# Performance work log

Hardware: AMD Instinct MI355X
Metric: run time of the kernel (lower is better)

The kernel has to match this reference:

```python
import jax, jax.numpy as jnp
import numpy as np

NB_CLASSES = 10
EPS = 1e-8  # torch cosine_similarity eps


def gcn_conv(x, W, b, src, dst, n):
    h = x @ W
    deg = jax.ops.segment_sum(jnp.ones_like(src, dtype=h.dtype), dst, num_segments=n) + 1.0
    dinv = deg ** -0.5
    coef = (dinv[src] * dinv[dst])[:, None]
    agg = jax.ops.segment_sum(h[src] * coef, dst, num_segments=n)
    return agg + h * (1.0 / deg)[:, None] + b


def condition_net(e, w_in, b_in, w_hid, b_hid, w_out, b_out):
    # ConditionNet with num_layers=2: input_fc -> elu -> hidden_fc[0] -> elu -> output_fc
    h = jax.nn.elu(e @ w_in + b_in)
    h = jax.nn.elu(h @ w_hid + b_hid)
    return h @ w_out + b_out


def setup_inputs() -> dict:
    key = jax.random.key(0)
    N, E, D, H, T, M = 20000, 320000, 256, 256, 3, 2048
    ks = jax.random.split(key, 24)
    s = 1.0 / np.sqrt(D)
    inp = {
        "x": jax.random.normal(ks[0], (N, D), dtype=jnp.float32),
        "src": jax.random.randint(ks[1], (E,), 0, N, dtype=jnp.int32),
        "dst": jax.random.randint(ks[2], (E,), 0, N, dtype=jnp.int32),
        "idx": jax.random.randint(ks[3], (M,), 0, N, dtype=jnp.int32),
        "labels": jax.random.randint(ks[4], (M,), 0, NB_CLASSES, dtype=jnp.int32),
        "train": 1,
        # 3 GCNConv layers (all D->D, residual structure forces equal widths)
        "gcn_W1": jax.random.normal(ks[5], (D, D), dtype=jnp.float32) * s,
        "gcn_b1": jnp.zeros((D,), dtype=jnp.float32),
        "gcn_W2": jax.random.normal(ks[6], (D, D), dtype=jnp.float32) * s,
        "gcn_b2": jnp.zeros((D,), dtype=jnp.float32),
        "gcn_W3": jax.random.normal(ks[7], (D, D), dtype=jnp.float32) * s,
        "gcn_b3": jnp.zeros((D,), dtype=jnp.float32),
        # T=3 ConditionNets, params stacked on leading axis
        "cn_w_in": jax.random.normal(ks[8], (T, D, H), dtype=jnp.float32) * s,
        "cn_b_in": jnp.zeros((T, H), dtype=jnp.float32),
        "cn_w_hid": jax.random.normal(ks[9], (T, H, H), dtype=jnp.float32) * s,
        "cn_b_hid": jnp.zeros((T, H), dtype=jnp.float32),
        "cn_w_out": jax.random.normal(ks[10], (T, H, D), dtype=jnp.float32) * s,
        "cn_b_out": jnp.zeros((T, D), dtype=jnp.float32),
        # Embed_prompt
        "p_list": jax.random.normal(ks[11], (5, D), dtype=jnp.float32) * s,
        "a_W": jax.random.normal(ks[12], (D, 5), dtype=jnp.float32) * s,
        "a_b": jnp.zeros((5,), dtype=jnp.float32),
        # gcn_weight2 (trainable); weight1 and weight3 are frozen zeros, closed over
        "gcn_weight2": jnp.float32(1.0),
    }
    return inp


def reference(x, src, dst, idx, labels, train,
              gcn_W1, gcn_b1, gcn_W2, gcn_b2, gcn_W3, gcn_b3,
              cn_w_in, cn_b_in, cn_w_hid, cn_b_hid, cn_w_out, cn_b_out,
              p_list, a_W, a_b, gcn_weight2):
    n = x.shape[0]
    origin_x = x
    w1 = jnp.float32(0.0)  # gcn_weight1 (frozen)
    w3 = jnp.float32(0.0)  # gcn_weight3 (frozen)
    T = cn_w_in.shape[0]
    for t in range(T):  # think layers (small static count)
        e1 = gcn_conv(x, gcn_W1, gcn_b1, src, dst, n)
        e2 = gcn_conv(e1, gcn_W2, gcn_b2, src, dst, n) + e1
        e3 = gcn_conv(e2, gcn_W3, gcn_b3, src, dst, n) + e2
        embed = w1 * e1 + gcn_weight2 * e2 + w3 * e3
        prompt = condition_net(embed, cn_w_in[t], cn_b_in[t], cn_w_hid[t], cn_b_hid[t],
                               cn_w_out[t], cn_b_out[t])
        x = prompt * origin_x
    # full gcn(x, edge_index): 3 convs with ELU activation (standard GCN forward)
    h = jax.nn.elu(gcn_conv(x, gcn_W1, gcn_b1, src, dst, n))
    h = jax.nn.elu(gcn_conv(h, gcn_W2, gcn_b2, src, dst, n))
    h = jax.nn.elu(gcn_conv(h, gcn_W3, gcn_b3, src, dst, n))
    # Embed_prompt: attention over 5 learned prompt vectors
    weight = jax.nn.softmax(h @ a_W + a_b, axis=1)  # [N, 5]
    embed = h + weight @ p_list
    rawret = embed[idx]  # [M, D]
    # train==1: class prototypes via scatter-mean over labels
    sums = jax.ops.segment_sum(rawret, labels, num_segments=NB_CLASSES)
    counts = jax.ops.segment_sum(jnp.ones_like(labels, dtype=rawret.dtype), labels,
                                 num_segments=NB_CLASSES)
    ave = sums / jnp.maximum(counts, 1.0)[:, None]  # [C, D]
    # fused cosine similarity: normalize both, one matmul (replaces M*C scalar loop)
    rn = rawret / jnp.maximum(jnp.linalg.norm(rawret, axis=1, keepdims=True), EPS)
    an = ave / jnp.maximum(jnp.linalg.norm(ave, axis=1, keepdims=True), EPS)
    ret = jax.nn.softmax(rn @ an.T, axis=1)  # [M, C]
    return ret
```

## Files before the change

### kernel.cpp

```cpp
#include <hip/hip_runtime.h>
#include <hip/hip_bf16.h>
#include <math.h>

#define NN 20000
#define DD 256
#define EE 320000
#define MM 2048
#define CC 10
#define TT 3

typedef __attribute__((ext_vector_type(8))) short s8v;
typedef __attribute__((ext_vector_type(4))) float f4v;

__device__ unsigned short g_xb[NN * DD];
__device__ unsigned short g_xo[NN * DD];
__device__ unsigned short g_hb[NN * DD];
__device__ unsigned short g_e1b[NN * DD];
__device__ unsigned short g_e2b[NN * DD];
__device__ int   g_cnt[NN];
__device__ int   g_cursor[NN];
__device__ int   g_rowstart[NN + 1];
__device__ float g_dinv[NN];
__device__ float g_invdeg[NN];
__device__ int   g_part[128];
__device__ int2  g_edge[EE];
__device__ float g_sums[CC * DD];
__device__ float g_cntf[CC];
__device__ unsigned short g_wT1[12 * DD * DD];
__device__ unsigned short g_wT2[12 * DD * DD];

__device__ __forceinline__ float wave_sum(float v) {
#pragma unroll
  for (int off = 32; off > 0; off >>= 1) v += __shfl_xor(v, off);
  return v;
}

__device__ __forceinline__ float eluf(float x) {
  return x > 0.f ? x : expm1f(x);
}

__device__ __forceinline__ float2 bfpair(unsigned int d) {
  union { unsigned int i; float f; } a, b;
  a.i = d << 16;
  b.i = d & 0xffff0000u;
  return make_float2(a.f, b.f);
}

__device__ __forceinline__ unsigned int packbf(float x, float y) {
  union { __hip_bfloat162 v; unsigned int u; } c;
  c.v = __float22bfloat162_rn(make_float2(x, y));
  return c.u;
}

__device__ __forceinline__ void gl_lds16(const unsigned short* g, unsigned short* l) {
  __builtin_amdgcn_global_load_lds(
      (const __attribute__((address_space(1))) unsigned int*)g,
      (__attribute__((address_space(3))) unsigned int*)l, 16, 0, 0);
}

struct WPtrs { const float* p[12]; };

__global__ __launch_bounds__(256) void init_k(const float* __restrict__ x,
                                              unsigned short* __restrict__ xb,
                                              WPtrs wp) {
  __shared__ float t[64][65];
  int b = blockIdx.x;
  int tid = threadIdx.x;
  if (b < 2500) {
    int i = b * 256 + tid;
    const float4* x4 = (const float4*)x;
    float4 a = x4[i * 2], bb = x4[i * 2 + 1];
    uint4 o;
    o.x = packbf(a.x, a.y);
    o.y = packbf(a.z, a.w);
    o.z = packbf(bb.x, bb.y);
    o.w = packbf(bb.z, bb.w);
    ((uint4*)xb)[i] = o;
  } else if (b < 2692) {
    int bb = b - 2500;
    int widx = bb >> 4;
    int rem = bb & 15;
    int kt0 = (rem >> 2) * 64, nt0 = (rem & 3) * 64;
    const float* W = wp.p[widx];
    int ln = tid & 63, lk = tid >> 6;
    for (int kk = lk; kk < 64; kk += 4)
      t[kk][ln] = W[(size_t)(kt0 + kk) * DD + nt0 + ln];
    __syncthreads();
    for (int nn = lk; nn < 64; nn += 4) {
      float v = t[ln][nn];
      __hip_bfloat16 hb = __float2bfloat16(v);
      float hf = __bfloat162float(hb);
      __hip_bfloat16 lb = __float2bfloat16(v - hf);
      union { __hip_bfloat16 b; unsigned short s; } ch, cl;
      ch.b = hb; cl.b = lb;
      size_t o = (size_t)widx * DD * DD + (size_t)(nt0 + nn) * DD + kt0 + ln;
      g_wT1[o] = ch.s;
      g_wT2[o] = cl.s;
    }
  } else {
    int i = (b - 2692) * 256 + tid;
    if (i < NN) { g_cnt[i] = 0; g_cursor[i] = 0; }
    if (i < CC * DD) g_sums[i] = 0.f;
    if (i < CC) g_cntf[i] = 0.f;
  }
}

__global__ void hist_k(const int* __restrict__ dst) {
  int e = blockIdx.x * blockDim.x + threadIdx.x;
  if (e < EE) atomicAdd(&g_cnt[dst[e]], 1);
}

__global__ __launch_bounds__(256) void scanA_k() {
  __shared__ int s[256];
  int t = threadIdx.x;
  int i = blockIdx.x * 256 + t;
  int v = (i < NN) ? g_cnt[i] : 0;
  s[t] = v;
  __syncthreads();
#pragma unroll
  for (int off = 128; off > 0; off >>= 1) {
    if (t < off) s[t] += s[t + off];
    __syncthreads();
  }
  if (t == 0) g_part[blockIdx.x] = s[0];
}

__global__ __launch_bounds__(256) void scanC_k() {
  __shared__ int ps[128];
  __shared__ int s[256];
  int t = threadIdx.x;
  if (t < 128) ps[t] = (t < 79) ? g_part[t] : 0;
  __syncthreads();
#pragma unroll
  for (int off = 1; off < 128; off <<= 1) {
    int v = (t >= off && t < 128) ? ps[t - off] : 0;
    __syncthreads();
    if (t < 128) ps[t] += v;
    __syncthreads();
  }
  int base = (blockIdx.x == 0) ? 0 : ps[blockIdx.x - 1];
  int i = blockIdx.x * 256 + t;
  int v = (i < NN) ? g_cnt[i] : 0;
  s[t] = v;
  __syncthreads();
#pragma unroll
  for (int off = 1; off < 256; off <<= 1) {
    int x2 = (t >= off) ? s[t - off] : 0;
    __syncthreads();
    s[t] += x2;
    __syncthreads();
  }
  if (i < NN) {
    g_rowstart[i] = base + s[t] - v;
    float dg = (float)(v + 1);
    g_invdeg[i] = 1.0f / dg;
    g_dinv[i] = 1.0f / sqrtf(dg);
  }
  if (blockIdx.x == 78 && t == 0) g_rowstart[NN] = EE;
}

__global__ void fill_k(const int* __restrict__ src, const int* __restrict__ dst) {
  int e = blockIdx.x * blockDim.x + threadIdx.x;
  if (e < EE) {
    int d = dst[e];
    int p = atomicAdd(&g_cursor[d], 1);
    int j = g_rowstart[d] + p;
    int si = src[e];
    float coef = g_dinv[si] * g_dinv[d];
    g_edge[j] = make_int2(si * 512, __float_as_int(coef));
  }
}

template <int SPLIT>
union GemmSM {
  unsigned short st[2][(1024 + 512 * SPLIT) * 8];
  float ct[64][68];
};

template <int EPI, int SPLIT>
__global__ __launch_bounds__(256) void gemm_k(const unsigned short* __restrict__ A,
                                              const unsigned short* __restrict__ B1,
                                              const unsigned short* __restrict__ B2,
                                              unsigned short* __restrict__ C,
                                              const float* __restrict__ bias,
                                              const float* __restrict__ alphap,
                                              const unsigned short* __restrict__ mul) {
  __shared__ GemmSM<SPLIT> sm;
  constexpr int CB = 1024 + 512 * SPLIT;
  int b = blockIdx.x;
  int xcd = b & 7, off = b >> 3;
  int logical = (xcd < 4) ? xcd * 157 + off : 628 + (xcd - 4) * 156 + off;
  int mblk = logical >> 2, nblk = logical & 3;
  int row0 = mblk * 64, col0 = nblk * 64;

  int tid = threadIdx.x;
  int wv = tid >> 6, lane = tid & 63;
  int wm = wv >> 1, wn = wv & 1;
  int lr = lane & 15, lk = lane >> 4;

  f4v acc[2][2];
#pragma unroll
  for (int i = 0; i < 2; ++i)
#pragma unroll
    for (int j = 0; j < 2; ++j) acc[i][j] = (f4v){0.f, 0.f, 0.f, 0.f};

  auto stage = [&](int buf, int kt) {
    unsigned short* base = sm.st[buf];
#pragma unroll
    for (int i = 0; i < CB / 256; ++i) {
      int cb = (wv * (CB / 256) + i) * 64;
      int c = cb + lane;
      unsigned short* ldst = base + (size_t)cb * 8;
      if (c < 512) {
        int row = c >> 3, pos = c & 7;
        int kc = pos ^ (row & 7);
        int gr = row0 + row;
        gr = gr < NN ? gr : NN - 1;
        gl_lds16(A + (size_t)gr * DD + kt + kc * 8, ldst);
      } else if (c < 1024) {
        int c2 = c - 512;
        int col = c2 >> 3, pos = c2 & 7;
        int kc = pos ^ (col & 7);
        gl_lds16(B1 + (size_t)(col0 + col) * DD + kt + kc * 8, ldst);
      } else {
        int c2 = c - 1024;
        int col = c2 >> 3, pos = c2 & 7;
        int kc = pos ^ (col & 7);
        gl_lds16(B2 + (size_t)(col0 + col) * DD + kt + kc * 8, ldst);
      }
    }
  };

  stage(0, 0);
  __syncthreads();

  int buf = 0;
#pragma unroll
  for (int t = 0; t < 4; ++t) {
    if (t < 3) stage(buf ^ 1, (t + 1) * 64);
    const unsigned short* base = sm.st[buf];
#pragma unroll
    for (int ksub = 0; ksub < 2; ++ksub) {
      int kc = ksub * 4 + lk;
      s8v a[2], b1v[2], b2v[2];
#pragma unroll
      for (int mi = 0; mi < 2; ++mi) {
        int row = wm * 32 + mi * 16 + lr;
        a[mi] = *(const s8v*)(base + (row * 8 + (kc ^ (row & 7))) * 8);
      }
#pragma unroll
      for (int nj = 0; nj < 2; ++nj) {
        int col = wn * 32 + nj * 16 + lr;
        int ch = col * 8 + (kc ^ (col & 7));
        b1v[nj] = *(const s8v*)(base + (512 + ch) * 8);
        if (SPLIT) b2v[nj] = *(const s8v*)(base + (1024 + ch) * 8);
      }
#pragma unroll
      for (int mi = 0; mi < 2; ++mi)
#pragma unroll
        for (int nj = 0; nj < 2; ++nj) {
          acc[mi][nj] = __builtin_amdgcn_mfma_f32_16x16x32_bf16(a[mi], b1v[nj], acc[mi][nj], 0, 0, 0);
          if (SPLIT)
            acc[mi][nj] = __builtin_amdgcn_mfma_f32_16x16x32_bf16(a[mi], b2v[nj], acc[mi][nj], 0, 0, 0);
        }
    }
    __syncthreads();
    buf ^= 1;
  }

#pragma unroll
  for (int mi = 0; mi < 2; ++mi)
#pragma unroll
    for (int nj = 0; nj < 2; ++nj)
#pragma unroll
      for (int r = 0; r < 4; ++r)
        sm.ct[wm * 32 + mi * 16 + lk * 4 + r][wn * 32 + nj * 16 + lr] = acc[mi][nj][r];
  __syncthreads();

  float alpha = 1.f;
  if (EPI == 1) alpha = alphap ? *alphap : 1.f;
#pragma unroll
  for (int p = 0; p < 2; ++p) {
    int row = p * 32 + (tid >> 3);
    int c0 = (tid & 7) * 8;
    int gr = row0 + row;
    int gc = col0 + c0;
    if (gr < NN) {
      float v[8];
      float4 va = *(float4*)&sm.ct[row][c0];
      float4 vb = *(float4*)&sm.ct[row][c0 + 4];
      v[0] = va.x; v[1] = va.y; v[2] = va.z; v[3] = va.w;
      v[4] = vb.x; v[5] = vb.y; v[6] = vb.z; v[7] = vb.w;
      if (EPI == 1) {
        float4 bv0 = *(const float4*)(bias + gc);
        float4 bv1 = *(const float4*)(bias + gc + 4);
        float bb[8] = {bv0.x, bv0.y, bv0.z, bv0.w, bv1.x, bv1.y, bv1.z, bv1.w};
#pragma unroll
        for (int i = 0; i < 8; ++i) v[i] = eluf(fmaf(alpha, v[i], bb[i]));
      } else if (EPI == 2) {
        float4 bv0 = *(const float4*)(bias + gc);
        float4 bv1 = *(const float4*)(bias + gc + 4);
        float bb[8] = {bv0.x, bv0.y, bv0.z, bv0.w, bv1.x, bv1.y, bv1.z, bv1.w};
        uint4 mu = *(const uint4*)(mul + (size_t)gr * DD + gc);
        float2 m0 = bfpair(mu.x), m1 = bfpair(mu.y), m2 = bfpair(mu.z), m3 = bfpair(mu.w);
        float mm[8] = {m0.x, m0.y, m1.x, m1.y, m2.x, m2.y, m3.x, m3.y};
#pragma unroll
        for (int i = 0; i < 8; ++i) v[i] = (v[i] + bb[i]) * mm[i];
      }
      uint4 o;
      o.x = packbf(v[0], v[1]);
      o.y = packbf(v[2], v[3]);
      o.z = packbf(v[4], v[5]);
      o.w = packbf(v[6], v[7]);
      *(uint4*)(C + (size_t)gr * DD + gc) = o;
    }
  }
}

template <int RES>
__device__ __forceinline__ void agg_row8(int row, int sl, int hf,
                                         const unsigned short* __restrict__ h,
                                         const float* __restrict__ bias,
                                         const unsigned short* __restrict__ res,
                                         float* o) {
  const char* hb = (const char*)h;
  int lo = sl * 16;
  float acc[8];
#pragma unroll
  for (int k = 0; k < 8; ++k) acc[k] = 0.f;
  int s = g_rowstart[row], e = g_rowstart[row + 1];
  int j = s;
  for (; j + 12 <= e; j += 12) {
    int2 E[6];
    uint4 V[6];
#pragma unroll
    for (int u = 0; u < 6; ++u) E[u] = g_edge[j + 2 * u + hf];
#pragma unroll
    for (int u = 0; u < 6; ++u) V[u] = *(const uint4*)(hb + (size_t)E[u].x + lo);
#pragma unroll
    for (int u = 0; u < 6; ++u) {
      float c = __int_as_float(E[u].y);
      float2 p0 = bfpair(V[u].x), p1 = bfpair(V[u].y);
      float2 p2 = bfpair(V[u].z), p3 = bfpair(V[u].w);
      acc[0] = fmaf(c, p0.x, acc[0]); acc[1] = fmaf(c, p0.y, acc[1]);
      acc[2] = fmaf(c, p1.x, acc[2]); acc[3] = fmaf(c, p1.y, acc[3]);
      acc[4] = fmaf(c, p2.x, acc[4]); acc[5] = fmaf(c, p2.y, acc[5]);
      acc[6] = fmaf(c, p3.x, acc[6]); acc[7] = fmaf(c, p3.y, acc[7]);
    }
  }
  if (j < e) {
    int2 E[6];
    uint4 V[6];
    int live[6];
#pragma unroll
    for (int u = 0; u < 6; ++u) {
      int jj = j + 2 * u + hf;
      live[u] = jj < e;
      E[u] = g_edge[live[u] ? jj : e - 1];
    }
#pragma unroll
    for (int u = 0; u < 6; ++u) V[u] = *(const uint4*)(hb + (size_t)E[u].x + lo);
#pragma unroll
    for (int u = 0; u < 6; ++u) {
      float c = live[u] ? __int_as_float(E[u].y) : 0.f;
      float2 p0 = bfpair(V[u].x), p1 = bfpair(V[u].y);
      float2 p2 = bfpair(V[u].z), p3 = bfpair(V[u].w);
      acc[0] = fmaf(c, p0.x, acc[0]); acc[1] = fmaf(c, p0.y, acc[1]);
      acc[2] = fmaf(c, p1.x, acc[2]); acc[3] = fmaf(c, p1.y, acc[3]);
      acc[4] = fmaf(c, p2.x, acc[4]); acc[5] = fmaf(c, p2.y, acc[5]);
      acc[6] = fmaf(c, p3.x, acc[6]); acc[7] = fmaf(c, p3.y, acc[7]);
    }
  }
#pragma unroll
  for (int k = 0; k < 8; ++k) acc[k] += __shfl_xor(acc[k], 32);
  float idg = g_invdeg[row];
  uint4 hv = *(const uint4*)(hb + (size_t)row * 512 + lo);
  float2 h0 = bfpair(hv.x), h1 = bfpair(hv.y), h2 = bfpair(hv.z), h3 = bfpair(hv.w);
  float hw[8] = {h0.x, h0.y, h1.x, h1.y, h2.x, h2.y, h3.x, h3.y};
  float4 b0 = *(const float4*)(bias + sl * 8);
  float4 b1 = *(const float4*)(bias + sl * 8 + 4);
  float bb[8] = {b0.x, b0.y, b0.z, b0.w, b1.x, b1.y, b1.z, b1.w};
#pragma unroll
  for (int k = 0; k < 8; ++k) o[k] = acc[k] + hw[k] * idg + bb[k];
  if (RES) {
    uint4 rv = *(const uint4*)((const char*)res + (size_t)row * 512 + lo);
    float2 r0 = bfpair(rv.x), r1 = bfpair(rv.y), r2 = bfpair(rv.z), r3 = bfpair(rv.w);
    float rw[8] = {r0.x, r0.y, r1.x, r1.y, r2.x, r2.y, r3.x, r3.y};
#pragma unroll
    for (int k = 0; k < 8; ++k) o[k] += rw[k];
  }
}

template <int ELU, int RES>
__global__ __launch_bounds__(256) void agg_k(const unsigned short* __restrict__ h,
                                             const float* __restrict__ bias,
                                             const unsigned short* __restrict__ res,
                                             unsigned short* __restrict__ out) {
  int row = (blockIdx.x * 256 + threadIdx.x) >> 6;
  int lane = threadIdx.x & 63;
  int sl = lane & 31, hf = lane >> 5;
  float o[8];
  agg_row8<RES>(row, sl, hf, h, bias, res, o);
  if (ELU) {
#pragma unroll
    for (int k = 0; k < 8; ++k) o[k] = eluf(o[k]);
  }
  if (hf == 0) {
    uint4 pk;
    pk.x = packbf(o[0], o[1]);
    pk.y = packbf(o[2], o[3]);
    pk.z = packbf(o[4], o[5]);
    pk.w = packbf(o[6], o[7]);
    *(uint4*)((char*)out + (size_t)row * 512 + sl * 16) = pk;
  }
}

__global__ __launch_bounds__(256) void agg_idx_k(const unsigned short* __restrict__ h,
                                                 const float* __restrict__ bias,
                                                 const int* __restrict__ idxp,
                                                 unsigned short* __restrict__ gath) {
  int m = (blockIdx.x * 256 + threadIdx.x) >> 6;
  int lane = threadIdx.x & 63;
  int sl = lane & 31, hf = lane >> 5;
  int row = idxp[m];
  float o[8];
  agg_row8<0>(row, sl, hf, h, bias, nullptr, o);
#pragma unroll
  for (int k = 0; k < 8; ++k) o[k] = eluf(o[k]);
  if (hf == 0) {
    uint4 pk;
    pk.x = packbf(o[0], o[1]);
    pk.y = packbf(o[2], o[3]);
    pk.z = packbf(o[4], o[5]);
    pk.w = packbf(o[6], o[7]);
    *(uint4*)((char*)gath + (size_t)m * 512 + sl * 16) = pk;
  }
}

__device__ __forceinline__ float4 attn_apply(float4 r, int lane,
                                             const float* __restrict__ aW,
                                             const float* __restrict__ ab,
                                             const float* __restrict__ plist) {
  int d = lane * 4;
  float lg[5];
#pragma unroll
  for (int k = 0; k < 5; ++k) {
    float p = r.x * aW[(d + 0) * 5 + k] + r.y * aW[(d + 1) * 5 + k] +
              r.z * aW[(d + 2) * 5 + k] + r.w * aW[(d + 3) * 5 + k];
    lg[k] = wave_sum(p) + ab[k];
  }
  float mx = lg[0];
#pragma unroll
  for (int k = 1; k < 5; ++k) mx = fmaxf(mx, lg[k]);
  float w[5], sum = 0.f;
#pragma unroll
  for (int k = 0; k < 5; ++k) { w[k] = expf(lg[k] - mx); sum += w[k]; }
  float inv = 1.f / sum;
#pragma unroll
  for (int k = 0; k < 5; ++k) {
    float wk = w[k] * inv;
    float4 pv = *(const float4*)(plist + k * DD + d);
    r.x = fmaf(wk, pv.x, r.x);
    r.y = fmaf(wk, pv.y, r.y);
    r.z = fmaf(wk, pv.z, r.z);
    r.w = fmaf(wk, pv.w, r.w);
  }
  return r;
}

__global__ __launch_bounds__(256) void proto_k(const unsigned short* __restrict__ gath,
                                               const int* __restrict__ labels,
                                               const float* __restrict__ aW,
                                               const float* __restrict__ ab,
                                               const float* __restrict__ plist) {
  __shared__ float sums[CC][DD];
  __shared__ float cnts[CC];
  int t = threadIdx.x;
#pragma unroll
  for (int c = 0; c < CC; ++c) sums[c][t] = 0.f;
  if (t < CC) cnts[t] = 0.f;
  __syncthreads();
  int wv = t >> 6, lane = t & 63;
  int m0 = blockIdx.x * 64 + wv * 16;
  int d = lane * 4;
  for (int rr = 0; rr < 16; ++rr) {
    int m = m0 + rr;
    int lab = labels[m];
    uint2 rv = *(const uint2*)((const char*)gath + (size_t)m * 512 + lane * 8);
    float2 a0 = bfpair(rv.x), a1 = bfpair(rv.y);
    float4 r = attn_apply(make_float4(a0.x, a0.y, a1.x, a1.y), lane, aW, ab, plist);
    atomicAdd(&sums[lab][d + 0], r.x);
    atomicAdd(&sums[lab][d + 1], r.y);
    atomicAdd(&sums[lab][d + 2], r.z);
    atomicAdd(&sums[lab][d + 3], r.w);
    if (lane == 0) atomicAdd(&cnts[lab], 1.f);
  }
  __syncthreads();
#pragma unroll
  for (int c = 0; c < CC; ++c) atomicAdd(&g_sums[c * DD + t], sums[c][t]);
  if (t < CC) atomicAdd(&g_cntf[t], cnts[t]);
}

__global__ __launch_bounds__(256) void cos_k(const unsigned short* __restrict__ gath,
                                             const float* __restrict__ aW,
                                             const float* __restrict__ ab,
                                             const float* __restrict__ plist,
                                             float* __restrict__ out) {
  __shared__ float an[CC][DD];
  __shared__ float red[4];
  int t = threadIdx.x;
  int lane = t & 63, wv = t >> 6;
  for (int c = 0; c < CC; ++c) {
    float v = g_sums[c * DD + t] / fmaxf(g_cntf[c], 1.0f);
    float sq = wave_sum(v * v);
    if (lane == 0) red[wv] = sq;
    __syncthreads();
    float tot = red[0] + red[1] + red[2] + red[3];
    float nrm = fmaxf(sqrtf(tot), 1e-8f);
    an[c][t] = v / nrm;
    __syncthreads();
  }
  int wid = (blockIdx.x * 256 + t) >> 6;
  if (wid >= MM) return;
  uint2 rv = *(const uint2*)((const char*)gath + (size_t)wid * 512 + lane * 8);
  float2 r0 = bfpair(rv.x), r1 = bfpair(rv.y);
  float4 r = attn_apply(make_float4(r0.x, r0.y, r1.x, r1.y), lane, aW, ab, plist);
  float n = wave_sum(r.x * r.x + r.y * r.y + r.z * r.z + r.w * r.w);
  float rnf = 1.0f / fmaxf(sqrtf(n), 1e-8f);
  float lg[CC];
#pragma unroll
  for (int c = 0; c < CC; ++c) {
    float4 a = ((const float4*)&an[c][0])[lane];
    float p = r.x * a.x + r.y * a.y + r.z * a.z + r.w * a.w;
    lg[c] = wave_sum(p) * rnf;
  }
  float mx = lg[0];
#pragma unroll
  for (int c = 1; c < CC; ++c) mx = fmaxf(mx, lg[c]);
  float s = 0.f, w[CC];
#pragma unroll
  for (int c = 0; c < CC; ++c) { w[c] = expf(lg[c] - mx); s += w[c]; }
  float inv = 1.f / s;
#pragma unroll
  for (int c = 0; c < CC; ++c)
    if (lane == c) out[(size_t)wid * CC + c] = w[c] * inv;
}

extern "C" void kernel_launch(void* const* d_in, const int* in_sizes, int n_in,
                              void* d_out, int out_size, void* d_ws, size_t ws_size,
                              hipStream_t stream) {
  (void)in_sizes; (void)n_in; (void)d_ws; (void)ws_size; (void)out_size;
  const float* x      = (const float*)d_in[0];
  const int*   src    = (const int*)d_in[1];
  const int*   dst    = (const int*)d_in[2];
  const int*   idx    = (const int*)d_in[3];
  const int*   labels = (const int*)d_in[4];
  const float* W1 = (const float*)d_in[6];
  const float* b1 = (const float*)d_in[7];
  const float* W2 = (const float*)d_in[8];
  const float* b2 = (const float*)d_in[9];
  const float* W3 = (const float*)d_in[10];
  const float* b3 = (const float*)d_in[11];
  const float* cw_in  = (const float*)d_in[12];
  const float* cb_in  = (const float*)d_in[13];
  const float* cw_hid = (const float*)d_in[14];
  const float* cb_hid = (const float*)d_in[15];
  const float* cw_out = (const float*)d_in[16];
  const float* cb_out = (const float*)d_in[17];
  const float* plist  = (const float*)d_in[18];
  const float* aW     = (const float*)d_in[19];
  const float* ab     = (const float*)d_in[20];
  const float* w2s    = (const float*)d_in[21];
  float* out = (float*)d_out;

  unsigned short *xb, *xo, *hb, *e1b, *e2b, *wt1, *wt2;
  hipGetSymbolAddress((void**)&xb,  HIP_SYMBOL(g_xb));
  hipGetSymbolAddress((void**)&xo,  HIP_SYMBOL(g_xo));
  hipGetSymbolAddress((void**)&hb,  HIP_SYMBOL(g_hb));
  hipGetSymbolAddress((void**)&e1b, HIP_SYMBOL(g_e1b));
  hipGetSymbolAddress((void**)&e2b, HIP_SYMBOL(g_e2b));
  hipGetSymbolAddress((void**)&wt1, HIP_SYMBOL(g_wT1));
  hipGetSymbolAddress((void**)&wt2, HIP_SYMBOL(g_wT2));

  auto WT1 = [&](int w) { return (const unsigned short*)(wt1 + (size_t)w * DD * DD); };
  auto WT2 = [&](int w) { return (const unsigned short*)(wt2 + (size_t)w * DD * DD); };

  WPtrs wp;
  wp.p[0] = W1; wp.p[1] = W2; wp.p[2] = W3;
  for (int t = 0; t < 3; ++t) {
    wp.p[3 + t] = cw_in  + (size_t)t * DD * DD;
    wp.p[6 + t] = cw_hid + (size_t)t * DD * DD;
    wp.p[9 + t] = cw_out + (size_t)t * DD * DD;
  }
  init_k<<<2771, 256, 0, stream>>>(x, xb, wp);
  hist_k<<<1250, 256, 0, stream>>>(dst);
  scanA_k<<<79, 256, 0, stream>>>();
  scanC_k<<<79, 256, 0, stream>>>();
  fill_k<<<1250, 256, 0, stream>>>(src, dst);

  const int GG = 1252;
  const unsigned short* xin = xb;
  for (int t = 0; t < TT; ++t) {
    gemm_k<0, 1><<<GG, 256, 0, stream>>>(xin, WT1(0), WT2(0), hb, nullptr, nullptr, nullptr);
    agg_k<0, 0><<<5000, 256, 0, stream>>>(hb, b1, nullptr, e1b);
    gemm_k<0, 1><<<GG, 256, 0, stream>>>(e1b, WT1(1), WT2(1), hb, nullptr, nullptr, nullptr);
    agg_k<0, 1><<<5000, 256, 0, stream>>>(hb, b2, e1b, e2b);
    gemm_k<1, 0><<<GG, 256, 0, stream>>>(e2b, WT1(3 + t), WT1(3 + t), e1b,
                                         cb_in + (size_t)t * DD, w2s, nullptr);
    gemm_k<1, 0><<<GG, 256, 0, stream>>>(e1b, WT1(6 + t), WT1(6 + t), hb,
                                         cb_hid + (size_t)t * DD, nullptr, nullptr);
    gemm_k<2, 0><<<GG, 256, 0, stream>>>(hb, WT1(9 + t), WT1(9 + t), xo,
                                         cb_out + (size_t)t * DD, nullptr, xb);
    xin = xo;
  }

  gemm_k<0, 1><<<GG, 256, 0, stream>>>(xin, WT1(0), WT2(0), hb, nullptr, nullptr, nullptr);
  agg_k<1, 0><<<5000, 256, 0, stream>>>(hb, b1, nullptr, e1b);
  gemm_k<0, 1><<<GG, 256, 0, stream>>>(e1b, WT1(1), WT2(1), hb, nullptr, nullptr, nullptr);
  agg_k<1, 0><<<5000, 256, 0, stream>>>(hb, b2, nullptr, e2b);
  gemm_k<0, 1><<<GG, 256, 0, stream>>>(e2b, WT1(2), WT2(2), hb, nullptr, nullptr, nullptr);
  agg_idx_k<<<512, 256, 0, stream>>>(hb, b3, idx, e1b);

  proto_k<<<32, 256, 0, stream>>>(e1b, labels, aW, ab, plist);
  cos_k<<<512, 256, 0, stream>>>(e1b, aW, ab, plist, out);
}
```

Baseline: 556.5 us.

## Merge scan kernels and software-pipeline edge index loads in aggregation

Folds the two-pass degree scan into one kernel in which each block recomputes all block partial sums itself from the count array, removing one launch and the partials buffer. The aggregation loop is restructured so the edge indices for the next 12-edge batch are loaded while the current batch's feature gathers and FMAs run, with the tail handled by masked coefficients in the same loop. This targets gather latency in the memory-bound aggregation. In exchange, every scan block redundantly reads the whole count array, and the aggregation uses more registers and always runs full masked batches.

After: 566.9 us. About the same (+1.9%).

```diff
diff --git a/kernel.cpp b/kernel.cpp
--- a/kernel.cpp
+++ b/kernel.cpp
@@ -22,7 +22,6 @@
 __device__ int   g_rowstart[NN + 1];
 __device__ float g_dinv[NN];
 __device__ float g_invdeg[NN];
-__device__ int   g_part[128];
 __device__ int2  g_edge[EE];
 __device__ float g_sums[CC * DD];
 __device__ float g_cntf[CC];
@@ -110,26 +109,29 @@
   if (e < EE) atomicAdd(&g_cnt[dst[e]], 1);
 }
 
-__global__ __launch_bounds__(256) void scanA_k() {
-  __shared__ int s[256];
-  int t = threadIdx.x;
-  int i = blockIdx.x * 256 + t;
-  int v = (i < NN) ? g_cnt[i] : 0;
-  s[t] = v;
-  __syncthreads();
-#pragma unroll
-  for (int off = 128; off > 0; off >>= 1) {
-    if (t < off) s[t] += s[t + off];
-    __syncthreads();
-  }
-  if (t == 0) g_part[blockIdx.x] = s[0];
-}
-
-__global__ __launch_bounds__(256) void scanC_k() {
+__global__ __launch_bounds__(256) void scan_k() {
   __shared__ int ps[128];
   __shared__ int s[256];
   int t = threadIdx.x;
-  if (t < 128) ps[t] = (t < 79) ? g_part[t] : 0;
+  if (t < 128) ps[t] = 0;
+  __syncthreads();
+  if (t < 79) {
+    const uint4* c4 = (const uint4*)g_cnt;
+    int base4 = t * 64;
+    int sum = 0;
+    for (int i = 0; i < 64; ++i) {
+      int idx = base4 + i;
+      if (idx * 4 < NN) {
+        uint4 v = c4[idx];
+        int lim = NN - idx * 4;
+        sum += (int)v.x;
+        if (lim > 1) sum += (int)v.y;
+        if (lim > 2) sum += (int)v.z;
+        if (lim > 3) sum += (int)v.w;
+      }
+    }
+    ps[t] = sum;
+  }
   __syncthreads();
 #pragma unroll
   for (int off = 1; off < 128; off <<= 1) {
@@ -329,46 +331,46 @@
 #pragma unroll
   for (int k = 0; k < 8; ++k) acc[k] = 0.f;
   int s = g_rowstart[row], e = g_rowstart[row + 1];
-  int j = s;
-  for (; j + 12 <= e; j += 12) {
+  int deg = e - s;
+  if (deg > 0) {
+    int nb = (deg + 11) / 12;
     int2 E[6];
-    uint4 V[6];
-#pragma unroll
-    for (int u = 0; u < 6; ++u) E[u] = g_edge[j + 2 * u + hf];
-#pragma unroll
-    for (int u = 0; u < 6; ++u) V[u] = *(const uint4*)(hb + (size_t)E[u].x + lo);
 #pragma unroll
     for (int u = 0; u < 6; ++u) {
-      float c = __int_as_float(E[u].y);
-      float2 p0 = bfpair(V[u].x), p1 = bfpair(V[u].y);
-      float2 p2 = bfpair(V[u].z), p3 = bfpair(V[u].w);
-      acc[0] = fmaf(c, p0.x, acc[0]); acc[1] = fmaf(c, p0.y, acc[1]);
-      acc[2] = fmaf(c, p1.x, acc[2]); acc[3] = fmaf(c, p1.y, acc[3]);
-      acc[4] = fmaf(c, p2.x, acc[4]); acc[5] = fmaf(c, p2.y, acc[5]);
-      acc[6] = fmaf(c, p3.x, acc[6]); acc[7] = fmaf(c, p3.y, acc[7]);
+      int jj = s + 2 * u + hf;
+      E[u] = g_edge[jj < e ? jj : e - 1];
     }
-  }
-  if (j < e) {
-    int2 E[6];
-    uint4 V[6];
-    int live[6];
-#pragma unroll
-    for (int u = 0; u < 6; ++u) {
-      int jj = j + 2 * u + hf;
-      live[u] = jj < e;
-      E[u] = g_edge[live[u] ? jj : e - 1];
-    }
-#pragma unroll
-    for (int u = 0; u < 6; ++u) V[u] = *(const uint4*)(hb + (size_t)E[u].x + lo);
-#pragma unroll
-    for (int u = 0; u < 6; ++u) {
-      float c = live[u] ? __int_as_float(E[u].y) : 0.f;
-      float2 p0 = bfpair(V[u].x), p1 = bfpair(V[u].y);
-      float2 p2 = bfpair(V[u].z), p3 = bfpair(V[u].w);
-      acc[0] = fmaf(c, p0.x, acc[0]); acc[1] = fmaf(c, p0.y, acc[1]);
-      acc[2] = fmaf(c, p1.x, acc[2]); acc[3] = fmaf(c, p1.y, acc[3]);
-      acc[4] = fmaf(c, p2.x, acc[4]); acc[5] = fmaf(c, p2.y, acc[5]);
-      acc[6] = fmaf(c, p3.x, acc[6]); acc[7] = fmaf(c, p3.y, acc[7]);
+#pragma unroll 1
+    for (int bi = 0; bi < nb; ++bi) {
+      uint4 V[6];
+#pragma unroll
+      for (int u = 0; u < 6; ++u) V[u] = *(const uint4*)(hb + (size_t)E[u].x + lo);
+      int2 En[6];
+      int prefetch = (bi + 1 < nb);
+      if (prefetch) {
+        int jb = s + (bi + 1) * 12;
+#pragma unroll
+        for (int u = 0; u < 6; ++u) {
+          int jj = jb + 2 * u + hf;
+          En[u] = g_edge[jj < e ? jj : e - 1];
+        }
+      }
+      int j0 = s + bi * 12;
+#pragma unroll
+      for (int u = 0; u < 6; ++u) {
+        int jj = j0 + 2 * u + hf;
+        float c = (jj < e) ? __int_as_float(E[u].y) : 0.f;
+        float2 p0 = bfpair(V[u].x), p1 = bfpair(V[u].y);
+        float2 p2 = bfpair(V[u].z), p3 = bfpair(V[u].w);
+        acc[0] = fmaf(c, p0.x, acc[0]); acc[1] = fmaf(c, p0.y, acc[1]);
+        acc[2] = fmaf(c, p1.x, acc[2]); acc[3] = fmaf(c, p1.y, acc[3]);
+        acc[4] = fmaf(c, p2.x, acc[4]); acc[5] = fmaf(c, p2.y, acc[5]);
+        acc[6] = fmaf(c, p3.x, acc[6]); acc[7] = fmaf(c, p3.y, acc[7]);
+      }
+      if (prefetch) {
+#pragma unroll
+        for (int u = 0; u < 6; ++u) E[u] = En[u];
+      }
     }
   }
 #pragma unroll
@@ -594,8 +596,7 @@
   }
   init_k<<<2771, 256, 0, stream>>>(x, xb, wp);
   hist_k<<<1250, 256, 0, stream>>>(dst);
-  scanA_k<<<79, 256, 0, stream>>>();
-  scanC_k<<<79, 256, 0, stream>>>();
+  scan_k<<<79, 256, 0, stream>>>();
   fill_k<<<1250, 256, 0, stream>>>(src, dst);
 
   const int GG = 1252;
```

## Fuse the whole GCN/ConditionNet pipeline into one persistent cooperative kernel

Applied to the files above, without the earlier changes.

Replaces about 30 separate GEMM, aggregation, prototype and cosine kernel launches with one cooperative persistent kernel. Each phase loops over its virtual blocks and is separated from the next by a software grid barrier built on atomic counters and a generation flag. The goal is to remove per-launch overhead and the idle gaps between small dependent kernels. It also merges the two-pass degree scan into a single kernel. The trade-offs are a grid limited by occupancy, a non-inlined GEMM body that can cost registers, and the barrier latency on every phase.

Result: slower. 2.011 ms (+261.4%).

```diff
diff --git a/kernel.cpp b/kernel.cpp
--- a/kernel.cpp
+++ b/kernel.cpp
@@ -22,12 +22,13 @@
 __device__ int   g_rowstart[NN + 1];
 __device__ float g_dinv[NN];
 __device__ float g_invdeg[NN];
-__device__ int   g_part[128];
 __device__ int2  g_edge[EE];
 __device__ float g_sums[CC * DD];
 __device__ float g_cntf[CC];
 __device__ unsigned short g_wT1[12 * DD * DD];
 __device__ unsigned short g_wT2[12 * DD * DD];
+__device__ int g_bar_cnt = 0;
+__device__ int g_bar_gen = 0;
 
 __device__ __forceinline__ float wave_sum(float v) {
 #pragma unroll
@@ -56,6 +57,24 @@
   __builtin_amdgcn_global_load_lds(
       (const __attribute__((address_space(1))) unsigned int*)g,
       (__attribute__((address_space(3))) unsigned int*)l, 16, 0, 0);
+}
+
+__device__ __forceinline__ void gsync() {
+  __syncthreads();
+  if (threadIdx.x == 0) {
+    __threadfence();
+    int gen = __hip_atomic_load(&g_bar_gen, __ATOMIC_RELAXED, __HIP_MEMORY_SCOPE_AGENT);
+    int a = __hip_atomic_fetch_add(&g_bar_cnt, 1, __ATOMIC_ACQ_REL, __HIP_MEMORY_SCOPE_AGENT);
+    if (a == (int)gridDim.x - 1) {
+      __hip_atomic_store(&g_bar_cnt, 0, __ATOMIC_RELAXED, __HIP_MEMORY_SCOPE_AGENT);
+      __hip_atomic_store(&g_bar_gen, gen + 1, __ATOMIC_RELEASE, __HIP_MEMORY_SCOPE_AGENT);
+    } else {
+      while (__hip_atomic_load(&g_bar_gen, __ATOMIC_ACQUIRE, __HIP_MEMORY_SCOPE_AGENT) == gen)
+        __builtin_amdgcn_s_sleep(8);
+    }
+    __threadfence();
+  }
+  __syncthreads();
 }
 
 struct WPtrs { const float* p[12]; };
@@ -110,26 +129,29 @@
   if (e < EE) atomicAdd(&g_cnt[dst[e]], 1);
 }
 
-__global__ __launch_bounds__(256) void scanA_k() {
-  __shared__ int s[256];
-  int t = threadIdx.x;
-  int i = blockIdx.x * 256 + t;
-  int v = (i < NN) ? g_cnt[i] : 0;
-  s[t] = v;
-  __syncthreads();
-#pragma unroll
-  for (int off = 128; off > 0; off >>= 1) {
-    if (t < off) s[t] += s[t + off];
-    __syncthreads();
-  }
-  if (t == 0) g_part[blockIdx.x] = s[0];
-}
-
-__global__ __launch_bounds__(256) void scanC_k() {
+__global__ __launch_bounds__(256) void scan_k() {
   __shared__ int ps[128];
   __shared__ int s[256];
   int t = threadIdx.x;
-  if (t < 128) ps[t] = (t < 79) ? g_part[t] : 0;
+  if (t < 128) ps[t] = 0;
+  __syncthreads();
+  if (t < 79) {
+    const uint4* c4 = (const uint4*)g_cnt;
+    int base4 = t * 64;
+    int sum = 0;
+    for (int i = 0; i < 64; ++i) {
+      int idx = base4 + i;
+      if (idx * 4 < NN) {
+        uint4 v = c4[idx];
+        int lim = NN - idx * 4;
+        sum += (int)v.x;
+        if (lim > 1) sum += (int)v.y;
+        if (lim > 2) sum += (int)v.z;
+        if (lim > 3) sum += (int)v.w;
+      }
+    }
+    ps[t] = sum;
+  }
   __syncthreads();
 #pragma unroll
   for (int off = 1; off < 128; off <<= 1) {
@@ -171,23 +193,19 @@
   }
 }
 
-template <int SPLIT>
-union GemmSM {
-  unsigned short st[2][(1024 + 512 * SPLIT) * 8];
+union MegaSM {
+  unsigned short st[2][1536 * 8];
   float ct[64][68];
+  struct { float sums[CC][DD]; float cnts[CC]; } proto;
+  struct { float an[CC][DD]; float red[4]; } cosm;
 };
 
 template <int EPI, int SPLIT>
-__global__ __launch_bounds__(256) void gemm_k(const unsigned short* __restrict__ A,
-                                              const unsigned short* __restrict__ B1,
-                                              const unsigned short* __restrict__ B2,
-                                              unsigned short* __restrict__ C,
-                                              const float* __restrict__ bias,
-                                              const float* __restrict__ alphap,
-                                              const unsigned short* __restrict__ mul) {
-  __shared__ GemmSM<SPLIT> sm;
+__device__ __attribute__((noinline)) void dev_gemm(
+    MegaSM& sm, const unsigned short* A, const unsigned short* B1,
+    const unsigned short* B2, unsigned short* C, const float* bias,
+    const float* alphap, const unsigned short* mul, int b) {
   constexpr int CB = 1024 + 512 * SPLIT;
-  int b = blockIdx.x;
   int xcd = b & 7, off = b >> 3;
   int logical = (xcd < 4) ? xcd * 157 + off : 628 + (xcd - 4) * 156 + off;
   int mblk = logical >> 2, nblk = logical & 3;
@@ -315,14 +333,21 @@
       *(uint4*)(C + (size_t)gr * DD + gc) = o;
     }
   }
+  __syncthreads();
+}
+
+template <int EPI, int SPLIT>
+__device__ void gemm_phase(MegaSM& sm, const unsigned short* A,
+                           const unsigned short* B1, const unsigned short* B2,
+                           unsigned short* C, const float* bias,
+                           const float* alphap, const unsigned short* mul) {
+  for (int vb = blockIdx.x; vb < 1252; vb += gridDim.x)
+    dev_gemm<EPI, SPLIT>(sm, A, B1, B2, C, bias, alphap, mul, vb);
 }
 
 template <int RES>
-__device__ __forceinline__ void agg_row8(int row, int sl, int hf,
-                                         const unsigned short* __restrict__ h,
-                                         const float* __restrict__ bias,
-                                         const unsigned short* __restrict__ res,
-                                         float* o) {
+__device__ void agg_row8(int row, int sl, int hf, const unsigned short* h,
+                         const float* bias, const unsigned short* res, float* o) {
   const char* hb = (const char*)h;
   int lo = sl * 16;
   float acc[8];
@@ -392,55 +417,51 @@
 }
 
 template <int ELU, int RES>
-__global__ __launch_bounds__(256) void agg_k(const unsigned short* __restrict__ h,
-                                             const float* __restrict__ bias,
-                                             const unsigned short* __restrict__ res,
-                                             unsigned short* __restrict__ out) {
-  int row = (blockIdx.x * 256 + threadIdx.x) >> 6;
-  int lane = threadIdx.x & 63;
+__device__ void agg_phase(const unsigned short* h, const float* bias,
+                          const unsigned short* res, unsigned short* out) {
+  int wv = threadIdx.x >> 6, lane = threadIdx.x & 63;
   int sl = lane & 31, hf = lane >> 5;
-  float o[8];
-  agg_row8<RES>(row, sl, hf, h, bias, res, o);
-  if (ELU) {
+  for (int row = blockIdx.x * 4 + wv; row < NN; row += gridDim.x * 4) {
+    float o[8];
+    agg_row8<RES>(row, sl, hf, h, bias, res, o);
+    if (ELU) {
+#pragma unroll
+      for (int k = 0; k < 8; ++k) o[k] = eluf(o[k]);
+    }
+    if (hf == 0) {
+      uint4 pk;
+      pk.x = packbf(o[0], o[1]);
+      pk.y = packbf(o[2], o[3]);
+      pk.z = packbf(o[4], o[5]);
+      pk.w = packbf(o[6], o[7]);
+      *(uint4*)((char*)out + (size_t)row * 512 + sl * 16) = pk;
+    }
+  }
+}
+
+__device__ void aggidx_phase(const unsigned short* h, const float* bias,
+                             const int* idxp, unsigned short* gath) {
+  int wv = threadIdx.x >> 6, lane = threadIdx.x & 63;
+  int sl = lane & 31, hf = lane >> 5;
+  for (int m = blockIdx.x * 4 + wv; m < MM; m += gridDim.x * 4) {
+    int row = idxp[m];
+    float o[8];
+    agg_row8<0>(row, sl, hf, h, bias, nullptr, o);
 #pragma unroll
     for (int k = 0; k < 8; ++k) o[k] = eluf(o[k]);
-  }
-  if (hf == 0) {
-    uint4 pk;
-    pk.x = packbf(o[0], o[1]);
-    pk.y = packbf(o[2], o[3]);
-    pk.z = packbf(o[4], o[5]);
-    pk.w = packbf(o[6], o[7]);
-    *(uint4*)((char*)out + (size_t)row * 512 + sl * 16) = pk;
-  }
-}
-
-__global__ __launch_bounds__(256) void agg_idx_k(const unsigned short* __restrict__ h,
-                                                 const float* __restrict__ bias,
-                                                 const int* __restrict__ idxp,
-                                                 unsigned short* __restrict__ gath) {
-  int m = (blockIdx.x * 256 + threadIdx.x) >> 6;
-  int lane = threadIdx.x & 63;
-  int sl = lane & 31, hf = lane >> 5;
-  int row = idxp[m];
-  float o[8];
-  agg_row8<0>(row, sl, hf, h, bias, nullptr, o);
-#pragma unroll
-  for (int k = 0; k < 8; ++k) o[k] = eluf(o[k]);
-  if (hf == 0) {
-    uint4 pk;
-    pk.x = packbf(o[0], o[1]);
-    pk.y = packbf(o[2], o[3]);
-    pk.z = packbf(o[4], o[5]);
-    pk.w = packbf(o[6], o[7]);
-    *(uint4*)((char*)gath + (size_t)m * 512 + sl * 16) = pk;
-  }
-}
-
-__device__ __forceinline__ float4 attn_apply(float4 r, int lane,
-                                             const float* __restrict__ aW,
-                                             const float* __restrict__ ab,
-                                             const float* __restrict__ plist) {
+    if (hf == 0) {
+      uint4 pk;
+      pk.x = packbf(o[0], o[1]);
+      pk.y = packbf(o[2], o[3]);
+      pk.z = packbf(o[4], o[5]);
+      pk.w = packbf(o[6], o[7]);
+      *(uint4*)((char*)gath + (size_t)m * 512 + sl * 16) = pk;
+    }
+  }
+}
+
+__device__ __forceinline__ float4 attn_apply(float4 r, int lane, const float* aW,
+                                             const float* ab, const float* plist) {
   int d = lane * 4;
   float lg[5];
 #pragma unroll
@@ -468,17 +489,14 @@
   return r;
 }
 
-__global__ __launch_bounds__(256) void proto_k(const unsigned short* __restrict__ gath,
-                                               const int* __restrict__ labels,
-                                               const float* __restrict__ aW,
-                                               const float* __restrict__ ab,
-                                               const float* __restrict__ plist) {
-  __shared__ float sums[CC][DD];
-  __shared__ float cnts[CC];
+__device__ void proto_phase(MegaSM& sm, const unsigned short* gath,
+                            const int* labels, const float* aW, const float* ab,
+                            const float* plist) {
+  if (blockIdx.x >= 32) return;
   int t = threadIdx.x;
 #pragma unroll
-  for (int c = 0; c < CC; ++c) sums[c][t] = 0.f;
-  if (t < CC) cnts[t] = 0.f;
+  for (int c = 0; c < CC; ++c) sm.proto.sums[c][t] = 0.f;
+  if (t < CC) sm.proto.cnts[t] = 0.f;
   __syncthreads();
   int wv = t >> 6, lane = t & 63;
   int m0 = blockIdx.x * 64 + wv * 16;
@@ -489,61 +507,116 @@
     uint2 rv = *(const uint2*)((const char*)gath + (size_t)m * 512 + lane * 8);
     float2 a0 = bfpair(rv.x), a1 = bfpair(rv.y);
     float4 r = attn_apply(make_float4(a0.x, a0.y, a1.x, a1.y), lane, aW, ab, plist);
-    atomicAdd(&sums[lab][d + 0], r.x);
-    atomicAdd(&sums[lab][d + 1], r.y);
-    atomicAdd(&sums[lab][d + 2], r.z);
-    atomicAdd(&sums[lab][d + 3], r.w);
-    if (lane == 0) atomicAdd(&cnts[lab], 1.f);
-  }
-  __syncthreads();
-#pragma unroll
-  for (int c = 0; c < CC; ++c) atomicAdd(&g_sums[c * DD + t], sums[c][t]);
-  if (t < CC) atomicAdd(&g_cntf[t], cnts[t]);
-}
-
-__global__ __launch_bounds__(256) void cos_k(const unsigned short* __restrict__ gath,
-                                             const float* __restrict__ aW,
-                                             const float* __restrict__ ab,
-                                             const float* __restrict__ plist,
-                                             float* __restrict__ out) {
-  __shared__ float an[CC][DD];
-  __shared__ float red[4];
+    atomicAdd(&sm.proto.sums[lab][d + 0], r.x);
+    atomicAdd(&sm.proto.sums[lab][d + 1], r.y);
+    atomicAdd(&sm.proto.sums[lab][d + 2], r.z);
+    atomicAdd(&sm.proto.sums[lab][d + 3], r.w);
+    if (lane == 0) atomicAdd(&sm.proto.cnts[lab], 1.f);
+  }
+  __syncthreads();
+#pragma unroll
+  for (int c = 0; c < CC; ++c) atomicAdd(&g_sums[c * DD + t], sm.proto.sums[c][t]);
+  if (t < CC) atomicAdd(&g_cntf[t], sm.proto.cnts[t]);
+}
+
+__device__ void cos_phase(MegaSM& sm, const unsigned short* gath, const float* aW,
+                          const float* ab, const float* plist, float* out) {
   int t = threadIdx.x;
   int lane = t & 63, wv = t >> 6;
-  for (int c = 0; c < CC; ++c) {
-    float v = g_sums[c * DD + t] / fmaxf(g_cntf[c], 1.0f);
-    float sq = wave_sum(v * v);
-    if (lane == 0) red[wv] = sq;
+  for (int vb = blockIdx.x; vb < 512; vb += gridDim.x) {
+    for (int c = 0; c < CC; ++c) {
+      float v = g_sums[c * DD + t] / fmaxf(g_cntf[c], 1.0f);
+      float sq = wave_sum(v * v);
+      if (lane == 0) sm.cosm.red[wv] = sq;
+      __syncthreads();
+      float tot = sm.cosm.red[0] + sm.cosm.red[1] + sm.cosm.red[2] + sm.cosm.red[3];
+      float nrm = fmaxf(sqrtf(tot), 1e-8f);
+      sm.cosm.an[c][t] = v / nrm;
+      __syncthreads();
+    }
+    int wid = vb * 4 + wv;
+    uint2 rv = *(const uint2*)((const char*)gath + (size_t)wid * 512 + lane * 8);
+    float2 r0 = bfpair(rv.x), r1 = bfpair(rv.y);
+    float4 r = attn_apply(make_float4(r0.x, r0.y, r1.x, r1.y), lane, aW, ab, plist);
+    float n = wave_sum(r.x * r.x + r.y * r.y + r.z * r.z + r.w * r.w);
+    float rnf = 1.0f / fmaxf(sqrtf(n), 1e-8f);
+    float lg[CC];
+#pragma unroll
+    for (int c = 0; c < CC; ++c) {
+      float4 a = ((const float4*)&sm.cosm.an[c][0])[lane];
+      float p = r.x * a.x + r.y * a.y + r.z * a.z + r.w * a.w;
+      lg[c] = wave_sum(p) * rnf;
+    }
+    float mx = lg[0];
+#pragma unroll
+    for (int c = 1; c < CC; ++c) mx = fmaxf(mx, lg[c]);
+    float s = 0.f, w[CC];
+#pragma unroll
+    for (int c = 0; c < CC; ++c) { w[c] = expf(lg[c] - mx); s += w[c]; }
+    float inv = 1.f / s;
+#pragma unroll
+    for (int c = 0; c < CC; ++c)
+      if (lane == c) out[(size_t)wid * CC + c] = w[c] * inv;
     __syncthreads();
-    float tot = red[0] + red[1] + red[2] + red[3];
-    float nrm = fmaxf(sqrtf(tot), 1e-8f);
-    an[c][t] = v / nrm;
-    __syncthreads();
-  }
-  int wid = (blockIdx.x * 256 + t) >> 6;
-  if (wid >= MM) return;
-  uint2 rv = *(const uint2*)((const char*)gath + (size_t)wid * 512 + lane * 8);
-  float2 r0 = bfpair(rv.x), r1 = bfpair(rv.y);
-  float4 r = attn_apply(make_float4(r0.x, r0.y, r1.x, r1.y), lane, aW, ab, plist);
-  float n = wave_sum(r.x * r.x + r.y * r.y + r.z * r.z + r.w * r.w);
-  float rnf = 1.0f / fmaxf(sqrtf(n), 1e-8f);
-  float lg[CC];
-#pragma unroll
-  for (int c = 0; c < CC; ++c) {
-    float4 a = ((const float4*)&an[c][0])[lane];
-    float p = r.x * a.x + r.y * a.y + r.z * a.z + r.w * a.w;
-    lg[c] = wave_sum(p) * rnf;
-  }
-  float mx = lg[0];
-#pragma unroll
-  for (int c = 1; c < CC; ++c) mx = fmaxf(mx, lg[c]);
-  float s = 0.f, w[CC];
-#pragma unroll
-  for (int c = 0; c < CC; ++c) { w[c] = expf(lg[c] - mx); s += w[c]; }
-  float inv = 1.f / s;
-#pragma unroll
-  for (int c = 0; c < CC; ++c)
-    if (lane == c) out[(size_t)wid * CC + c] = w[c] * inv;
+  }
+}
+
+struct MainArgs {
+  const unsigned short* xb;
+  unsigned short *xo, *hb, *e1b, *e2b;
+  const unsigned short *wt1, *wt2;
+  const float *b1, *b2, *b3;
+  const float *cb_in, *cb_hid, *cb_out;
+  const float *w2s;
+  const int *idx, *labels;
+  const float *aW, *ab, *plist;
+  float* out;
+};
+
+__global__ __launch_bounds__(256) void main_k(MainArgs a) {
+  __shared__ MegaSM sm;
+  const unsigned short* wt1 = a.wt1;
+  const unsigned short* wt2 = a.wt2;
+  const unsigned short* xin = a.xb;
+#pragma unroll 1
+  for (int t = 0; t < TT; ++t) {
+    gemm_phase<0, 1>(sm, xin, wt1, wt2, a.hb, nullptr, nullptr, nullptr);
+    gsync();
+    agg_phase<0, 0>(a.hb, a.b1, nullptr, a.e1b);
+    gsync();
+    gemm_phase<0, 1>(sm, a.e1b, wt1 + DD * DD, wt2 + DD * DD, a.hb,
+                     nullptr, nullptr, nullptr);
+    gsync();
+    agg_phase<0, 1>(a.hb, a.b2, a.e1b, a.e2b);
+    gsync();
+    gemm_phase<1, 0>(sm, a.e2b, wt1 + (size_t)(3 + t) * DD * DD, nullptr, a.e1b,
+                     a.cb_in + (size_t)t * DD, a.w2s, nullptr);
+    gsync();
+    gemm_phase<1, 0>(sm, a.e1b, wt1 + (size_t)(6 + t) * DD * DD, nullptr, a.hb,
+                     a.cb_hid + (size_t)t * DD, nullptr, nullptr);
+    gsync();
+    gemm_phase<2, 0>(sm, a.hb, wt1 + (size_t)(9 + t) * DD * DD, nullptr, a.xo,
+                     a.cb_out + (size_t)t * DD, nullptr, a.xb);
+    gsync();
+    xin = a.xo;
+  }
+  gemm_phase<0, 1>(sm, xin, wt1, wt2, a.hb, nullptr, nullptr, nullptr);
+  gsync();
+  agg_phase<1, 0>(a.hb, a.b1, nullptr, a.e1b);
+  gsync();
+  gemm_phase<0, 1>(sm, a.e1b, wt1 + DD * DD, wt2 + DD * DD, a.hb,
+                   nullptr, nullptr, nullptr);
+  gsync();
+  agg_phase<1, 0>(a.hb, a.b2, nullptr, a.e2b);
+  gsync();
+  gemm_phase<0, 1>(sm, a.e2b, wt1 + 2 * DD * DD, wt2 + 2 * DD * DD, a.hb,
+                   nullptr, nullptr, nullptr);
+  gsync();
+  aggidx_phase(a.hb, a.b3, a.idx, a.e1b);
+  gsync();
+  proto_phase(sm, a.e1b, a.labels, a.aW, a.ab, a.plist);
+  gsync();
+  cos_phase(sm, a.e1b, a.aW, a.ab, a.plist, a.out);
 }
 
 extern "C" void kernel_launch(void* const* d_in, const int* in_sizes, int n_in,
@@ -574,16 +647,13 @@
   float* out = (float*)d_out;
 
   unsigned short *xb, *xo, *hb, *e1b, *e2b, *wt1, *wt2;
-  hipGetSymbolAddress((void**)&xb,  HIP_SYMBOL(g_xb));
-  hipGetSymbolAddress((void**)&xo,  HIP_SYMBOL(g_xo));
-  hipGetSymbolAddress((void**)&hb,  HIP_SYMBOL(g_hb));
-  hipGetSymbolAddress((void**)&e1b, HIP_SYMBOL(g_e1b));
-  hipGetSymbolAddress((void**)&e2b, HIP_SYMBOL(g_e2b));
-  hipGetSymbolAddress((void**)&wt1, HIP_SYMBOL(g_wT1));
-  hipGetSymbolAddress((void**)&wt2, HIP_SYMBOL(g_wT2));
-
-  auto WT1 = [&](int w) { return (const unsigned short*)(wt1 + (size_t)w * DD * DD); };
-  auto WT2 = [&](int w) { return (const unsigned short*)(wt2 + (size_t)w * DD * DD); };
+  (void)hipGetSymbolAddress((void**)&xb,  HIP_SYMBOL(g_xb));
+  (void)hipGetSymbolAddress((void**)&xo,  HIP_SYMBOL(g_xo));
+  (void)hipGetSymbolAddress((void**)&hb,  HIP_SYMBOL(g_hb));
+  (void)hipGetSymbolAddress((void**)&e1b, HIP_SYMBOL(g_e1b));
+  (void)hipGetSymbolAddress((void**)&e2b, HIP_SYMBOL(g_e2b));
+  (void)hipGetSymbolAddress((void**)&wt1, HIP_SYMBOL(g_wT1));
+  (void)hipGetSymbolAddress((void**)&wt2, HIP_SYMBOL(g_wT2));
 
   WPtrs wp;
   wp.p[0] = W1; wp.p[1] = W2; wp.p[2] = W3;
@@ -594,33 +664,22 @@
   }
   init_k<<<2771, 256, 0, stream>>>(x, xb, wp);
   hist_k<<<1250, 256, 0, stream>>>(dst);
-  scanA_k<<<79, 256, 0, stream>>>();
-  scanC_k<<<79, 256, 0, stream>>>();
+  scan_k<<<79, 256, 0, stream>>>();
   fill_k<<<1250, 256, 0, stream>>>(src, dst);
 
-  const int GG = 1252;
-  const unsigned short* xin = xb;
-  for (int t = 0; t < TT; ++t) {
-    gemm_k<0, 1><<<GG, 256, 0, stream>>>(xin, WT1(0), WT2(0), hb, nullptr, nullptr, nullptr);
-    agg_k<0, 0><<<5000, 256, 0, stream>>>(hb, b1, nullptr, e1b);
-    gemm_k<0, 1><<<GG, 256, 0, stream>>>(e1b, WT1(1), WT2(1), hb, nullptr, nullptr, nullptr);
-    agg_k<0, 1><<<5000, 256, 0, stream>>>(hb, b2, e1b, e2b);
-    gemm_k<1, 0><<<GG, 256, 0, stream>>>(e2b, WT1(3 + t), WT1(3 + t), e1b,
-                                         cb_in + (size_t)t * DD, w2s, nullptr);
-    gemm_k<1, 0><<<GG, 256, 0, stream>>>(e1b, WT1(6 + t), WT1(6 + t), hb,
-                                         cb_hid + (size_t)t * DD, nullptr, nullptr);
-    gemm_k<2, 0><<<GG, 256, 0, stream>>>(hb, WT1(9 + t), WT1(9 + t), xo,
-                                         cb_out + (size_t)t * DD, nullptr, xb);
-    xin = xo;
-  }
-
-  gemm_k<0, 1><<<GG, 256, 0, stream>>>(xin, WT1(0), WT2(0), hb, nullptr, nullptr, nullptr);
-  agg_k<1, 0><<<5000, 256, 0, stream>>>(hb, b1, nullptr, e1b);
-  gemm_k<0, 1><<<GG, 256, 0, stream>>>(e1b, WT1(1), WT2(1), hb, nullptr, nullptr, nullptr);
-  agg_k<1, 0><<<5000, 256, 0, stream>>>(hb, b2, nullptr, e2b);
-  gemm_k<0, 1><<<GG, 256, 0, stream>>>(e2b, WT1(2), WT2(2), hb, nullptr, nullptr, nullptr);
-  agg_idx_k<<<512, 256, 0, stream>>>(hb, b3, idx, e1b);
-
-  proto_k<<<32, 256, 0, stream>>>(e1b, labels, aW, ab, plist);
-  cos_k<<<512, 256, 0, stream>>>(e1b, aW, ab, plist, out);
-}
+  MainArgs ma;
+  ma.xb = xb; ma.xo = xo; ma.hb = hb; ma.e1b = e1b; ma.e2b = e2b;
+  ma.wt1 = wt1; ma.wt2 = wt2;
+  ma.b1 = b1; ma.b2 = b2; ma.b3 = b3;
+  ma.cb_in = cb_in; ma.cb_hid = cb_hid; ma.cb_out = cb_out;
+  ma.w2s = w2s; ma.idx = idx; ma.labels = labels;
+  ma.aW = aW; ma.ab = ab; ma.plist = plist; ma.out = out;
+
+  int occ = 0;
+  (void)hipOccupancyMaxActiveBlocksPerMultiprocessor(&occ, (const void*)main_k, 256, 0);
+  if (occ < 1) occ = 1;
+  if (occ > 3) occ = 3;
+  int grid = occ * 256;
+  void* kargs[] = {&ma};
+  (void)hipLaunchCooperativeKernel((void*)main_k, dim3(grid), dim3(256), kargs, 0, stream);
+}
```
